# Kernel optimization log

Measured on AMD Instinct MI355X. Metric: run time of the kernel, lower is better.

## Reference

```python
import jax, jax.numpy as jnp
import numpy as np

RES = 200        # self.res, hard-coded in the module
MODES_OUT = 16
MODES_IN = 32
T_SEQ = 10
D_MODEL = 256
BATCH = 16


def setup_inputs() -> dict:
    key = jax.random.key(0)
    k1, k2, k3 = jax.random.split(key, 3)
    v = jax.random.normal(k1, (BATCH, T_SEQ, D_MODEL, 2, MODES_IN), dtype=jnp.float32)
    scale = 1.0 / (MODES_IN * MODES_OUT)
    # weights1 = scale * rand(T,1,1,mo,mi) cfloat; singleton dims broadcast -> store as [T,mo,mi]
    w_real = scale * jax.random.uniform(k2, (T_SEQ, MODES_OUT, MODES_IN), dtype=jnp.float32)
    w_imag = scale * jax.random.uniform(k3, (T_SEQ, MODES_OUT, MODES_IN), dtype=jnp.float32)
    return {"v": v, "w_real": w_real, "w_imag": w_imag}


def reference(v, w_real, w_imag):
    # v: [B,T,H,2,mi] -> complex x_ft = r + i*1j
    r = v[:, :, :, 0, :]  # [B,T,H,mi]
    i = v[:, :, :, 1, :]
    # einsum 'bthix,thiox->bthox' with h=i=1 in weights == broadcast complex multiply
    wr = w_real[None, :, None, :, :]  # [1,T,1,mo,mi]
    wi = w_imag[None, :, None, :, :]
    rr = r[:, :, :, None, :]          # [B,T,H,1,mi]
    ii = i[:, :, :, None, :]
    re = rr * wr - ii * wi            # [B,T,H,mo,mi] = Re(out_ft)
    im = rr * wi + ii * wr            # Im(out_ft)
    amp = jax.nn.relu(jnp.sqrt(re * re + im * im))  # relu(|out_ft|)
    ph = jnp.arctan2(im, re)                          # angle(out_ft)
    # cosine reconstruction grid: theta[o,x] = 2*pi*f_o*x, f from fftfreq(res, d=1/(res-1))
    x_res = jnp.linspace(0.0, 1.0, RES).astype(jnp.float32)
    dx = x_res[1] - x_res[0]
    freqs = jnp.fft.fftfreq(RES, d=dx)[:MODES_OUT].astype(jnp.float32)  # [mo]
    theta = (2.0 * jnp.pi) * freqs[:, None] * x_res[None, :]            # [mo,res]
    # sum over mi of amp*cos(theta + ph) = cos(theta)*sum(amp*cos ph) - sin(theta)*sum(amp*sin ph)
    # (exact trig identity; avoids materializing the 6-D [B,T,H,mo,mi,res] tensor)
    C = jnp.sum(amp * jnp.cos(ph), axis=-1)  # [B,T,H,mo]
    S = jnp.sum(amp * jnp.sin(ph), axis=-1)  # [B,T,H,mo]
    out = (jnp.einsum('btho,ox->btxh', C, jnp.cos(theta))
           - jnp.einsum('btho,ox->btxh', S, jnp.sin(theta)))  # [B,T,res,H]
    return out
```

## Files before the change

kernel.cpp:

```cpp
#include <hip/hip_runtime.h>

#define B_   16
#define T_   10
#define D_   256
#define MI_  32
#define MO_  16
#define RES_ 200
#define TWO_PI 6.28318530717958647692f

#define HSLICE 32
#define NHS    (D_ / HSLICE)
#define VPAD   68
#define BT_STRIDE (2 * MO_ * D_)
#define CS_BYTES ((size_t)B_ * T_ * BT_STRIDE * sizeof(float))

using f32x4 = __attribute__((ext_vector_type(4))) float;

__global__ __launch_bounds__(256) void spectral_cs(
    const float* __restrict__ v,
    const float* __restrict__ w_real,
    const float* __restrict__ w_imag,
    float* __restrict__ ws)
{
    const int blk = blockIdx.x;
    const int bt  = blk >> 3;
    const int hs  = blk & 7;
    const int t   = bt % T_;

    __shared__ float s_v[HSLICE * VPAD];

    {
        const float4* gv = reinterpret_cast<const float4*>(
            v + ((size_t)bt * D_ + hs * HSLICE) * (2 * MI_));
        #pragma unroll
        for (int j = 0; j < 2; ++j) {
            const int f = threadIdx.x + 256 * j;
            const int h = f >> 4;
            const int m = (f & 15) * 4;
            *reinterpret_cast<float4*>(&s_v[h * VPAD + m]) = gv[f];
        }
    }
    __syncthreads();

    const int og  = threadIdx.x >> 5;
    const int h_l = threadIdx.x & 31;
    const int o0  = og * 2;
    const int h_g = hs * HSLICE + h_l;

    float rr[MI_], ii[MI_];
    #pragma unroll
    for (int j = 0; j < 8; ++j) {
        float4 q = *reinterpret_cast<const float4*>(&s_v[h_l * VPAD + 4 * j]);
        rr[4*j+0]=q.x; rr[4*j+1]=q.y; rr[4*j+2]=q.z; rr[4*j+3]=q.w;
    }
    #pragma unroll
    for (int j = 0; j < 8; ++j) {
        float4 q = *reinterpret_cast<const float4*>(&s_v[h_l * VPAD + 32 + 4 * j]);
        ii[4*j+0]=q.x; ii[4*j+1]=q.y; ii[4*j+2]=q.z; ii[4*j+3]=q.w;
    }

    const float* wrt = w_real + ((size_t)t * MO_ + o0) * MI_;
    const float* wit = w_imag + ((size_t)t * MO_ + o0) * MI_;

    float* wsb = ws + (size_t)bt * BT_STRIDE;
    #pragma unroll
    for (int ol = 0; ol < 2; ++ol) {
        const float4* wa = reinterpret_cast<const float4*>(wrt + ol * MI_);
        const float4* wb = reinterpret_cast<const float4*>(wit + ol * MI_);
        float c = 0.f, s = 0.f;
        #pragma unroll
        for (int mq = 0; mq < 8; ++mq) {
            float4 a4 = wa[mq];
            float4 b4 = wb[mq];
            c = fmaf(rr[4*mq+0], a4.x, c); c = fmaf(-ii[4*mq+0], b4.x, c);
            s = fmaf(rr[4*mq+0], b4.x, s); s = fmaf( ii[4*mq+0], a4.x, s);
            c = fmaf(rr[4*mq+1], a4.y, c); c = fmaf(-ii[4*mq+1], b4.y, c);
            s = fmaf(rr[4*mq+1], b4.y, s); s = fmaf( ii[4*mq+1], a4.y, s);
            c = fmaf(rr[4*mq+2], a4.z, c); c = fmaf(-ii[4*mq+2], b4.z, c);
            s = fmaf(rr[4*mq+2], b4.z, s); s = fmaf( ii[4*mq+2], a4.z, s);
            c = fmaf(rr[4*mq+3], a4.w, c); c = fmaf(-ii[4*mq+3], b4.w, c);
            s = fmaf(rr[4*mq+3], b4.w, s); s = fmaf( ii[4*mq+3], a4.w, s);
        }
        const int o = o0 + ol;
        wsb[o * D_ + h_g]              = c;
        wsb[MO_ * D_ + o * D_ + h_g]   = s;
    }
}

__global__ __launch_bounds__(256) void spectral_ift(
    const float* __restrict__ ws,
    float* __restrict__ out)
{
    const int blk  = blockIdx.x;
    const int bt   = blk >> 2;
    const int qb   = blk & 3;
    const int wave = threadIdx.x >> 6;
    const int lane = threadIdx.x & 63;
    const int g    = qb * 4 + wave;
    const int h0   = lane * 4;

    const float* wsb = ws + (size_t)bt * BT_STRIDE;
    float C[MO_][4], S[MO_][4];
    #pragma unroll
    for (int o = 0; o < MO_; ++o) {
        float4 c4 = *reinterpret_cast<const float4*>(&wsb[o * D_ + h0]);
        float4 s4 = *reinterpret_cast<const float4*>(&wsb[MO_ * D_ + o * D_ + h0]);
        C[o][0]=c4.x; C[o][1]=c4.y; C[o][2]=c4.z; C[o][3]=c4.w;
        S[o][0]=s4.x; S[o][1]=s4.y; S[o][2]=s4.z; S[o][3]=s4.w;
    }

    float* ob = out + (size_t)bt * RES_ * D_;

    #pragma unroll
    for (int k = 0; k < 7; ++k) {
        const int s = g + 16 * k;
        if (s <= 100) {
            const float phi = (float)s * (TWO_PI / (float)RES_);
            float s1, c1;
            __sincosf(phi, &s1, &c1);

            float a0=0.f,a1=0.f,a2=0.f,a3=0.f;
            float b0=0.f,b1=0.f,b2=0.f,b3=0.f;
            float co = 1.f, so = 0.f;
            #pragma unroll
            for (int o = 0; o < MO_; ++o) {
                a0 = fmaf(C[o][0], co, a0);
                a1 = fmaf(C[o][1], co, a1);
                a2 = fmaf(C[o][2], co, a2);
                a3 = fmaf(C[o][3], co, a3);
                b0 = fmaf(S[o][0], so, b0);
                b1 = fmaf(S[o][1], so, b1);
                b2 = fmaf(S[o][2], so, b2);
                b3 = fmaf(S[o][3], so, b3);
                const float nc = fmaf(co, c1, -(so * s1));
                const float ns = fmaf(so, c1,  (co * s1));
                co = nc; so = ns;
            }

            const int mr = (s == 0) ? 0 : (RES_ - s);
            f32x4 lo, hi;
            lo.x = a0 - b0; lo.y = a1 - b1; lo.z = a2 - b2; lo.w = a3 - b3;
            hi.x = a0 + b0; hi.y = a1 + b1; hi.z = a2 + b2; hi.w = a3 + b3;
            __builtin_nontemporal_store(
                lo, reinterpret_cast<f32x4*>(&ob[(size_t)s  * D_ + h0]));
            __builtin_nontemporal_store(
                hi, reinterpret_cast<f32x4*>(&ob[(size_t)mr * D_ + h0]));
        }
    }
}

extern "C" void kernel_launch(void* const* d_in, const int* in_sizes, int n_in,
                              void* d_out, int out_size, void* d_ws, size_t ws_size,
                              hipStream_t stream) {
    const float* v  = (const float*)d_in[0];
    const float* wr = (const float*)d_in[1];
    const float* wi = (const float*)d_in[2];
    float* out = (float*)d_out;
    float* ws  = (float*)d_ws;

    spectral_cs <<<B_ * T_ * NHS, 256, 0, stream>>>(v, wr, wi, ws);
    spectral_ift<<<B_ * T_ * 4,   256, 0, stream>>>(ws, out);
}
```

Before: 24.79 us.

## Precompute twiddle table in extra blocks and double IFT grid parallelism

Extra blocks appended to the first kernel compute a cos/sin table for every (slot, mode) pair into workspace. The IFT kernel loads that table into shared memory and reads twiddles from it, replacing the per-slot sincos and the rotation recurrence. The IFT grid doubles from 4 to 8 blocks per (b,t), so each wave handles fewer slots. The cost is a shared-memory load plus a barrier in every block, and each block reloads the same C/S coefficients, now across twice as many blocks.

```diff
diff --git a/kernel.cpp b/kernel.cpp
--- a/kernel.cpp
+++ b/kernel.cpp
@@ -12,7 +12,11 @@
 #define NHS    (D_ / HSLICE)
 #define VPAD   68
 #define BT_STRIDE (2 * MO_ * D_)
-#define CS_BYTES ((size_t)B_ * T_ * BT_STRIDE * sizeof(float))
+#define NSLOT  101
+#define TRIG_OFF ((size_t)B_ * T_ * BT_STRIDE)
+#define TRIG_FLOATS (NSLOT * 2 * MO_)
+#define TRIG_BLOCKS 7
+#define WS_FLOATS (TRIG_OFF + TRIG_FLOATS)
 
 using f32x4 = __attribute__((ext_vector_type(4))) float;
 
@@ -23,6 +27,23 @@
     float* __restrict__ ws)
 {
     const int blk = blockIdx.x;
+
+    if (blk >= B_ * T_ * NHS) {
+        const int p = (blk - B_ * T_ * NHS) * 256 + threadIdx.x;
+        if (p < NSLOT * MO_) {
+            const int s = p >> 4;
+            const int o = p & 15;
+            const int k = (s * o) % RES_;
+            float ang = TWO_PI * ((float)k * (1.0f / (float)RES_));
+            float sv, cv;
+            __sincosf(ang, &sv, &cv);
+            float* tt = ws + TRIG_OFF;
+            tt[2 * p]     = cv;
+            tt[2 * p + 1] = sv;
+        }
+        return;
+    }
+
     const int bt  = blk >> 3;
     const int hs  = blk & 7;
     const int t   = bt % T_;
@@ -82,8 +103,8 @@
             s = fmaf(rr[4*mq+3], b4.w, s); s = fmaf( ii[4*mq+3], a4.w, s);
         }
         const int o = o0 + ol;
-        wsb[o * D_ + h_g]              = c;
-        wsb[MO_ * D_ + o * D_ + h_g]   = s;
+        wsb[o * D_ + h_g]            = c;
+        wsb[MO_ * D_ + o * D_ + h_g] = s;
     }
 }
 
@@ -92,12 +113,24 @@
     float* __restrict__ out)
 {
     const int blk  = blockIdx.x;
-    const int bt   = blk >> 2;
-    const int qb   = blk & 3;
+    const int bt   = blk >> 3;
+    const int qb   = blk & 7;
     const int wave = threadIdx.x >> 6;
     const int lane = threadIdx.x & 63;
     const int g    = qb * 4 + wave;
     const int h0   = lane * 4;
+
+    __shared__ float s_tt[TRIG_FLOATS];
+
+    {
+        const float4* gt4 = reinterpret_cast<const float4*>(ws + TRIG_OFF);
+        #pragma unroll
+        for (int i = 0; i < 4; ++i) {
+            const int idx = threadIdx.x + 256 * i;
+            if (idx < TRIG_FLOATS / 4)
+                reinterpret_cast<float4*>(s_tt)[idx] = gt4[idx];
+        }
+    }
 
     const float* wsb = ws + (size_t)bt * BT_STRIDE;
     float C[MO_][4], S[MO_][4];
@@ -108,35 +141,29 @@
         C[o][0]=c4.x; C[o][1]=c4.y; C[o][2]=c4.z; C[o][3]=c4.w;
         S[o][0]=s4.x; S[o][1]=s4.y; S[o][2]=s4.z; S[o][3]=s4.w;
     }
+    __syncthreads();
 
     float* ob = out + (size_t)bt * RES_ * D_;
 
     #pragma unroll
-    for (int k = 0; k < 7; ++k) {
-        const int s = g + 16 * k;
+    for (int k = 0; k < 4; ++k) {
+        const int s = g + 32 * k;
         if (s <= 100) {
-            const float phi = (float)s * (TWO_PI / (float)RES_);
-            float s1, c1;
-            __sincosf(phi, &s1, &c1);
-
+            const float* tp = &s_tt[s * 2 * MO_];
             float a0=0.f,a1=0.f,a2=0.f,a3=0.f;
             float b0=0.f,b1=0.f,b2=0.f,b3=0.f;
-            float co = 1.f, so = 0.f;
             #pragma unroll
             for (int o = 0; o < MO_; ++o) {
-                a0 = fmaf(C[o][0], co, a0);
-                a1 = fmaf(C[o][1], co, a1);
-                a2 = fmaf(C[o][2], co, a2);
-                a3 = fmaf(C[o][3], co, a3);
-                b0 = fmaf(S[o][0], so, b0);
-                b1 = fmaf(S[o][1], so, b1);
-                b2 = fmaf(S[o][2], so, b2);
-                b3 = fmaf(S[o][3], so, b3);
-                const float nc = fmaf(co, c1, -(so * s1));
-                const float ns = fmaf(so, c1,  (co * s1));
-                co = nc; so = ns;
+                float2 tv = *reinterpret_cast<const float2*>(&tp[2 * o]);
+                a0 = fmaf(C[o][0], tv.x, a0);
+                a1 = fmaf(C[o][1], tv.x, a1);
+                a2 = fmaf(C[o][2], tv.x, a2);
+                a3 = fmaf(C[o][3], tv.x, a3);
+                b0 = fmaf(S[o][0], tv.y, b0);
+                b1 = fmaf(S[o][1], tv.y, b1);
+                b2 = fmaf(S[o][2], tv.y, b2);
+                b3 = fmaf(S[o][3], tv.y, b3);
             }
-
             const int mr = (s == 0) ? 0 : (RES_ - s);
             f32x4 lo, hi;
             lo.x = a0 - b0; lo.y = a1 - b1; lo.z = a2 - b2; lo.w = a3 - b3;
@@ -158,6 +185,6 @@
     float* out = (float*)d_out;
     float* ws  = (float*)d_ws;
 
-    spectral_cs <<<B_ * T_ * NHS, 256, 0, stream>>>(v, wr, wi, ws);
-    spectral_ift<<<B_ * T_ * 4,   256, 0, stream>>>(ws, out);
+    spectral_cs <<<B_ * T_ * NHS + TRIG_BLOCKS, 256, 0, stream>>>(v, wr, wi, ws);
+    spectral_ift<<<B_ * T_ * 8,                 256, 0, stream>>>(ws, out);
 }
```

Measured after the change: 31.15 us. 1.26x slower.
